# Kernel optimization log

Hardware: AMD Instinct MI355X
Metric: run time of the kernel (lower is better)

The kernel has to match this reference:

```python
import jax, jax.numpy as jnp
import numpy as np

DEPTH, HEADS, DIM_HEAD = 6, 8, 64
B, N, E = 2, 128, 160
NUM_ATOMS, NF = 100, 127
DIM = NF + 1                 # 128, node feature dim fed to transformer
INNER = HEADS * DIM_HEAD     # 512


def setup_inputs() -> dict:
    key = jax.random.key(0)
    ks = iter(jax.random.split(key, 40))
    f32 = jnp.float32
    def w(shape, scale=0.02):
        return jax.random.normal(next(ks), shape, dtype=f32) * scale
    inp = {
        "indices": jax.random.randint(next(ks), (B, N), 0, NUM_ATOMS),
        "coordinates": jax.random.normal(next(ks), (B, N, 3), dtype=f32),
        "bonds": jax.random.randint(next(ks), (E, 2), 0, N),
        "noise_level": jax.random.uniform(next(ks), (1,), dtype=f32),
        "atom_emb": w((NUM_ATOMS, NF), 1.0),
        "ln1_g": jnp.ones((DEPTH, DIM), f32), "ln1_b": jnp.zeros((DEPTH, DIM), f32),
        "Wq": w((DEPTH, DIM, INNER)), "bq": jnp.zeros((DEPTH, INNER), f32),
        "Wkv": w((DEPTH, DIM, 2 * INNER)), "bkv": jnp.zeros((DEPTH, 2 * INNER), f32),
        "We": w((DEPTH, 3, INNER)), "be": jnp.zeros((DEPTH, INNER), f32),
        "Wo": w((DEPTH, INNER, DIM)), "bo": jnp.zeros((DEPTH, DIM), f32),
        "Wg1": w((DEPTH, 3 * DIM, 1)),
        "ln2_g": jnp.ones((DEPTH, DIM), f32), "ln2_b": jnp.zeros((DEPTH, DIM), f32),
        "W1": w((DEPTH, DIM, 4 * DIM)), "b1": jnp.zeros((DEPTH, 4 * DIM), f32),
        "W2": w((DEPTH, 4 * DIM, DIM)), "b2": jnp.zeros((DEPTH, DIM), f32),
        "Wg2": w((DEPTH, 3 * DIM, 1)),
        "Wlin": w((DIM, 1)), "blin": jnp.zeros((1,), f32),
    }
    return inp


def _ln(x, g, b, eps=1e-5):
    m = jnp.mean(x, -1, keepdims=True)
    v = jnp.mean((x - m) ** 2, -1, keepdims=True)
    return (x - m) * jax.lax.rsqrt(v + eps) * g + b


def _gated_residual(x, res, Wg):
    # gate = sigmoid(Linear([x, res, x-res])); out = x*gate + res*(1-gate)
    gate = jax.nn.sigmoid(jnp.concatenate([x, res, x - res], -1) @ Wg)  # (B,N,1)
    return x * gate + res * (1.0 - gate)


def _forward(indices, bonds, coordinates, noise_level, atom_emb,
             ln1_g, ln1_b, Wq, bq, Wkv, bkv, We, be, Wo, bo, Wg1,
             ln2_g, ln2_b, W1, b1, W2, b2, Wg2, Wlin, blin):
    b, n = indices.shape
    # nodes_embedding: atom embedding + noise-level channel
    noise = jnp.broadcast_to(noise_level.reshape(1, 1, 1).astype(coordinates.dtype), (b, n, 1))
    nodes = jnp.concatenate([atom_emb[indices], noise], -1)  # (B,N,DIM)
    # edges_embedding: vectorized scatter of per-bond coordinate differences
    i, j = bonds[:, 0], bonds[:, 1]
    diff = coordinates[:, i] - coordinates[:, j]             # (B,E,3)
    edges = jnp.zeros((b, n, n, 3), coordinates.dtype)
    edges = edges.at[:, i, j].set(diff).at[:, j, i].set(-diff)

    scale = DIM_HEAD ** -0.5
    for l in range(DEPTH):
        # PreNorm + edge-biased attention (mask is all-ones -> no-op)
        xn = _ln(nodes, ln1_g[l], ln1_b[l])
        q = (xn @ Wq[l] + bq[l]).reshape(b, n, HEADS, DIM_HEAD)
        k, v = jnp.split(xn @ Wkv[l] + bkv[l], 2, -1)
        k = k.reshape(b, n, HEADS, DIM_HEAD)
        v = v.reshape(b, n, HEADS, DIM_HEAD)
        e = (edges @ We[l] + be[l]).reshape(b, n, n, HEADS, DIM_HEAD)
        kk = k[:, None] + e                                   # (B,i,j,H,D)
        vv = v[:, None] + e
        sim = jnp.einsum('bihd,bijhd->bijh', q, kk) * scale
        attn = jax.nn.softmax(sim, axis=2)                    # softmax over j
        out = jnp.einsum('bijh,bijhd->bihd', attn, vv).reshape(b, n, INNER)
        out = out @ Wo[l] + bo[l]
        nodes = _gated_residual(out, nodes, Wg1[l])
        # PreNorm + FeedForward (exact GELU, mult=4) + gated residual
        xn = _ln(nodes, ln2_g[l], ln2_b[l])
        ff = jax.nn.gelu(xn @ W1[l] + b1[l], approximate=False) @ W2[l] + b2[l]
        nodes = _gated_residual(ff, nodes, Wg2[l])
    return jnp.sum(nodes @ Wlin + blin)


def reference(indices, coordinates, bonds, noise_level, atom_emb,
              ln1_g, ln1_b, Wq, bq, Wkv, bkv, We, be, Wo, bo, Wg1,
              ln2_g, ln2_b, W1, b1, W2, b2, Wg2, Wlin, blin):
    return _forward(indices, bonds, coordinates, noise_level, atom_emb,
                    ln1_g, ln1_b, Wq, bq, Wkv, bkv, We, be, Wo, bo, Wg1,
                    ln2_g, ln2_b, W1, b1, W2, b2, Wg2, Wlin, blin)
```

## Files before the change

### kernel.cpp

```cpp
#include <hip/hip_runtime.h>
#include <hip/hip_fp16.h>
#include <math.h>

#define DEPTH 6
#define HEADS 8
#define BB    2
#define NN    128
#define EE    160
#define NF    127
#define DIMM  128
#define INNER 512
#define NNODE 256

__device__ __forceinline__ void gload16(const void* g, void* l) {
    __builtin_amdgcn_global_load_lds((const __attribute__((address_space(1))) void*)g,
                                     (__attribute__((address_space(3))) void*)l,
                                     16, 0, 0);
}

__device__ __forceinline__ void wait_vm0() { __builtin_amdgcn_s_waitcnt(0x0f70); }
__device__ __forceinline__ void wait_lgkm0() { __builtin_amdgcn_s_waitcnt(0xC07F); }

__device__ __forceinline__ void wstage16(const char* gslice, char* ldsslice, int ln) {
#pragma unroll
    for (int i = 0; i < 16; i++)
        gload16(gslice + i * 1024 + ln * 16, ldsslice + i * 1024);
}
__device__ __forceinline__ void wstage16s(const char* gslice, int rowstride,
                                          char* ldsslice, int ln) {
#pragma unroll
    for (int i = 0; i < 16; i++)
        gload16(gslice + (size_t)i * rowstride + ln * 16, ldsslice + i * 1024);
}

__device__ __forceinline__ void fma8h(float4& a0, float4& a1, float s, float4 raw) {
    const __half2* hp = (const __half2*)&raw;
    float2 p0 = __half22float2(hp[0]), p1 = __half22float2(hp[1]);
    float2 p2 = __half22float2(hp[2]), p3 = __half22float2(hp[3]);
    a0.x += s * p0.x; a0.y += s * p0.y; a0.z += s * p1.x; a0.w += s * p1.y;
    a1.x += s * p2.x; a1.y += s * p2.y; a1.z += s * p3.x; a1.w += s * p3.y;
}

__device__ __forceinline__ void gemv512(const float* act, const float* wbuf,
                                        float* s_part, int w, int ln) {
    float4 a0 = {0,0,0,0}, a1 = {0,0,0,0};
    const float4* w4 = (const float4*)wbuf;
#pragma unroll
    for (int r = 0; r < 16; r++)
        fma8h(a0, a1, act[w * 16 + r], w4[r * 64 + ln]);
    ((float4*)(s_part + w * 512))[ln * 2]     = a0;
    ((float4*)(s_part + w * 512))[ln * 2 + 1] = a1;
}

__device__ __forceinline__ void gemv128(const float* act, const float* wbuf,
                                        float* s_part, int w, int ln) {
    float2 acc = {0, 0};
#pragma unroll 8
    for (int r = 0; r < 64; r++) {
        float raw = wbuf[r * 64 + ln];
        __half2 h = *(__half2*)&raw;
        float2 p = __half22float2(h);
        float a = act[w * 64 + r];
        acc.x += a * p.x; acc.y += a * p.y;
    }
    s_part[w * 128 + ln * 2]     = acc.x;
    s_part[w * 128 + ln * 2 + 1] = acc.y;
}

__device__ __forceinline__ float block_reduce_sum_8w(float val, float* sbuf) {
#pragma unroll
    for (int off = 32; off > 0; off >>= 1) val += __shfl_xor(val, off, 64);
    int wave = threadIdx.x >> 6;
    if ((threadIdx.x & 63) == 0) sbuf[wave] = val;
    __syncthreads();
    float r = sbuf[0] + sbuf[1] + sbuf[2] + sbuf[3] + sbuf[4] + sbuf[5] + sbuf[6] + sbuf[7];
    __syncthreads();
    return r;
}

__device__ __forceinline__ float2 block_reduce_sum2_8w(float a, float b, float* sbuf16) {
#pragma unroll
    for (int off = 32; off > 0; off >>= 1) {
        a += __shfl_xor(a, off, 64);
        b += __shfl_xor(b, off, 64);
    }
    int wave = threadIdx.x >> 6;
    if ((threadIdx.x & 63) == 0) { sbuf16[2 * wave] = a; sbuf16[2 * wave + 1] = b; }
    __syncthreads();
    float ra = 0.0f, rb = 0.0f;
#pragma unroll
    for (int g = 0; g < 8; g++) { ra += sbuf16[2 * g]; rb += sbuf16[2 * g + 1]; }
    __syncthreads();
    float2 r; r.x = ra; r.y = rb;
    return r;
}


__global__ __launch_bounds__(512) void k_cvt(const float* Wq, const float* Wkv,
                                             const float* Wo, const float* W1,
                                             const float* W2,
                                             __half* hWq, __half* hWkv, __half* hWo,
                                             __half* hW1, __half* hW2,
                                             const float* blin, float* out) {
    if (blockIdx.x == 0 && threadIdx.x == 0) out[0] = 256.0f * blin[0];
    int g = blockIdx.x * 512 + threadIdx.x;
    const float4* src; __half* dst; int off;
    if (g < 98304)       { src = (const float4*)Wq;  dst = hWq;  off = g; }
    else if (g < 294912) { src = (const float4*)Wkv; dst = hWkv; off = g - 98304; }
    else if (g < 393216) { src = (const float4*)Wo;  dst = hWo;  off = g - 294912; }
    else if (g < 491520) { src = (const float4*)W1;  dst = hW1;  off = g - 393216; }
    else                 { src = (const float4*)W2;  dst = hW2;  off = g - 491520; }
    float4 v = src[off];
    __half2* d2 = (__half2*)(dst + (size_t)off * 4);
    d2[0] = __floats2half2_rn(v.x, v.y);
    d2[1] = __floats2half2_rn(v.z, v.w);
}

__global__ __launch_bounds__(512, 1) void k_pre(const int* indices, const float* noise,
                                                const float* atom_emb,
                                                const float* ln1_g, const float* ln1_b,
                                                const __half* hWq, const float* bq,
                                                const __half* hWkv, const float* bkv,
                                                float* nodes, float* qb,
                                                __half* hk, __half* hv) {
    int bn = blockIdx.x;
    int t  = threadIdx.x;
    int d  = t & 127;
    bool own = (t < 128);
    int w = t >> 6, ln = t & 63;
    __shared__ float arena[32768];
    __shared__ float s_xn[128];
    __shared__ float s_red[16];
    __shared__ float s_part[4096];
    char*  lslice = (char*)arena + w * 16384;
    float* wbuf   = arena + w * 4096;

    const char* WqL  = (const char*)(hWq + 0);
    const char* WkvL = (const char*)(hWkv + 0);
    wstage16(WqL + w * 16384, lslice, ln);

    float nd = 0.0f;
    if (own) {
        int idx = indices[bn];
        nd = (d < NF) ? atom_emb[idx * NF + d] : noise[0];
        nodes[bn * DIMM + d] = nd;
    }
    float2 ss = block_reduce_sum2_8w(own ? nd : 0.0f, own ? nd * nd : 0.0f, s_red);
    float m   = ss.x * (1.0f / 128.0f);
    float var = ss.y * (1.0f / 128.0f) - m * m;
    if (own) s_xn[d] = (nd - m) * rsqrtf(var + 1e-5f) * ln1_g[d] + ln1_b[d];
    __syncthreads();

    wait_vm0();
    gemv512(s_xn, wbuf, s_part, w, ln);
    wait_lgkm0();
    wstage16s(WkvL + (size_t)(w * 16) * 2048, 2048, lslice, ln);
    __syncthreads();
    {
        float q = bq[t];
#pragma unroll
        for (int g = 0; g < 8; g++) q += s_part[g * 512 + t];
        qb[(size_t)bn * INNER + t] = q;
    }
    __syncthreads();

    wait_vm0();
    gemv512(s_xn, wbuf, s_part, w, ln);
    wait_lgkm0();
    wstage16s(WkvL + (size_t)(w * 16) * 2048 + 1024, 2048, lslice, ln);
    __syncthreads();
    {
        float k = bkv[t];
#pragma unroll
        for (int g = 0; g < 8; g++) k += s_part[g * 512 + t];
        hk[(size_t)bn * INNER + t] = __float2half(k);
    }
    __syncthreads();

    wait_vm0();
    gemv512(s_xn, wbuf, s_part, w, ln);
    __syncthreads();
    {
        float v = bkv[INNER + t];
#pragma unroll
        for (int g = 0; g < 8; g++) v += s_part[g * 512 + t];
        hv[(size_t)bn * INNER + t] = __float2half(v);
    }
}

__global__ __launch_bounds__(512, 1) void k_layer(int l,
        const float* coords, const int* bonds,
        const float* We, const float* be,
        float* qb, const __half* hkin, const __half* hvin,
        __half* hkout, __half* hvout,
        const __half* hWo, const float* bo, const float* Wg1,
        const float* ln2_g, const float* ln2_b,
        const __half* hW1, const float* b1,
        const __half* hW2, const float* b2,
        const float* Wg2,
        const float* ln1_g, const float* ln1_b,
        const __half* hWq, const float* bq,
        const __half* hWkv, const float* bkv,
        float* nodes, const float* Wlin, float* out) {
    int bn = blockIdx.x;
    int b = bn >> 7, i = bn & 127;
    int t = threadIdx.x;
    int d = t & 127;
    bool own = (t < 128);
    int w = t >> 6, ln = t & 63;

    __shared__ float arena[32768];
    __shared__ float scoord[384];
    __shared__ float sedge[384];
    __shared__ int   sadj[128];
    __shared__ float s_l[64];
    __shared__ float s_ao[512];
    __shared__ float s_h[512];
    __shared__ float s_xn[128];
    __shared__ float s_red[16];
    __shared__ float s_part[4096];
    float* s_o = s_part;
    char*  lslice = (char*)arena + w * 16384;
    float* wbuf   = arena + w * 4096;

    const char* WoL  = (const char*)(hWo + (size_t)l * INNER * DIMM);
    const char* W1L  = (const char*)(hW1 + (size_t)l * DIMM * 4 * DIMM);
    const char* W2L  = (const char*)(hW2 + (size_t)l * 4 * DIMM * DIMM);
    const char* WqL  = (const char*)(hWq + (size_t)(l + 1) * DIMM * INNER);
    const char* WkvL = (const char*)(hWkv + (size_t)(l + 1) * DIMM * 2 * INNER);

    wstage16(WoL + w * 16384, lslice, ln);

    const float4* qR4 = (const float4*)(qb + (size_t)bn * INNER);
    const float4* WeR = (const float4*)(We + (size_t)l * 3 * INNER);
    float4 qa  = qR4[ln * 2],        qz  = qR4[ln * 2 + 1];
    float4 w0a = WeR[ln * 2],        w0z = WeR[ln * 2 + 1];
    float4 w1a = WeR[128 + ln * 2],  w1z = WeR[129 + ln * 2];
    float4 w2a = WeR[256 + ln * 2],  w2z = WeR[257 + ln * 2];
    float4 bea = ((const float4*)(be + (size_t)l * INNER))[ln * 2];
    float4 bez = ((const float4*)(be + (size_t)l * INNER))[ln * 2 + 1];
    float res = own ? nodes[bn * DIMM + d] : 0.0f;

    if (t < 3 * NN) scoord[t] = coords[b * 3 * NN + t];
    if (t < NN) sadj[t] = 0;
    __syncthreads();
    if (t < EE) {
        int e0 = bonds[2 * t], e1 = bonds[2 * t + 1];
        if (e0 == i) sadj[e1] = 1;
        if (e1 == i) sadj[e0] = 1;
    }
    __syncthreads();
    if (t < NN) {
        int j = t;
        float msk = sadj[j] ? 1.0f : 0.0f;
        sedge[3 * j + 0] = msk * (scoord[3 * i + 0] - scoord[3 * j + 0]);
        sedge[3 * j + 1] = msk * (scoord[3 * i + 1] - scoord[3 * j + 1]);
        sedge[3 * j + 2] = msk * (scoord[3 * i + 2] - scoord[3 * j + 2]);
    }
    __syncthreads();

    const float4* kR = (const float4*)(hkin + (size_t)b * NN * INNER);
    const float4* vR = (const float4*)(hvin + (size_t)b * NN * INNER);
    float l_run = 0.0f;
    float4 o0 = {0, 0, 0, 0}, o1 = {0, 0, 0, 0};
    int j0 = w * 16;
#pragma unroll
    for (int base = 0; base < 16; base += 4) {
        float4 kraw[4], vraw[4];
#pragma unroll
        for (int p = 0; p < 4; p++) {
            int j = j0 + base + p;
            kraw[p] = kR[j * 64 + ln];
            vraw[p] = vR[j * 64 + ln];
        }
#pragma unroll
        for (int p = 0; p < 4; p++) {
            int j = j0 + base + p;
            float ex = sedge[3 * j], ey = sedge[3 * j + 1], ez = sedge[3 * j + 2];
            float4 e0, e1;
            e0.x = bea.x + ex * w0a.x + ey * w1a.x + ez * w2a.x;
            e0.y = bea.y + ex * w0a.y + ey * w1a.y + ez * w2a.y;
            e0.z = bea.z + ex * w0a.z + ey * w1a.z + ez * w2a.z;
            e0.w = bea.w + ex * w0a.w + ey * w1a.w + ez * w2a.w;
            e1.x = bez.x + ex * w0z.x + ey * w1z.x + ez * w2z.x;
            e1.y = bez.y + ex * w0z.y + ey * w1z.y + ez * w2z.y;
            e1.z = bez.z + ex * w0z.z + ey * w1z.z + ez * w2z.z;
            e1.w = bez.w + ex * w0z.w + ey * w1z.w + ez * w2z.w;
            const __half2* kh = (const __half2*)&kraw[p];
            float2 k0 = __half22float2(kh[0]), k1 = __half22float2(kh[1]);
            float2 k2 = __half22float2(kh[2]), k3 = __half22float2(kh[3]);
            float s = qa.x * (k0.x + e0.x) + qa.y * (k0.y + e0.y)
                    + qa.z * (k1.x + e0.z) + qa.w * (k1.y + e0.w)
                    + qz.x * (k2.x + e1.x) + qz.y * (k2.y + e1.y)
                    + qz.z * (k3.x + e1.z) + qz.w * (k3.y + e1.w);
            s += __shfl_xor(s, 1, 64);
            s += __shfl_xor(s, 2, 64);
            s += __shfl_xor(s, 4, 64);
            float pp = __expf(s * 0.125f);
            const __half2* vh = (const __half2*)&vraw[p];
            float2 v0 = __half22float2(vh[0]), v1 = __half22float2(vh[1]);
            float2 v2 = __half22float2(vh[2]), v3 = __half22float2(vh[3]);
            l_run += pp;
            o0.x += pp * (v0.x + e0.x); o0.y += pp * (v0.y + e0.y);
            o0.z += pp * (v1.x + e0.z); o0.w += pp * (v1.y + e0.w);
            o1.x += pp * (v2.x + e1.x); o1.y += pp * (v2.y + e1.y);
            o1.z += pp * (v3.x + e1.z); o1.w += pp * (v3.y + e1.w);
        }
    }
    ((float4*)(s_o + w * 512))[ln * 2]     = o0;
    ((float4*)(s_o + w * 512))[ln * 2 + 1] = o1;
    if ((ln & 7) == 0) s_l[w * 8 + (ln >> 3)] = l_run;
    __syncthreads();
    {
        float o = 0.0f;
#pragma unroll
        for (int g = 0; g < 8; g++) o += s_o[g * 512 + t];
        int h = t >> 6;
        float lsum = 0.0f;
#pragma unroll
        for (int g = 0; g < 8; g++) lsum += s_l[g * 8 + h];
        s_ao[t] = o / lsum;
    }
    __syncthreads();

    wait_vm0();
    gemv128(s_ao, wbuf, s_part, w, ln);
    wait_lgkm0();
    wstage16(W1L + w * 16384, lslice, ln);
    __syncthreads();
    float x = 0.0f;
    if (own) {
        x = bo[l * DIMM + d];
#pragma unroll
        for (int g = 0; g < 8; g++) x += s_part[g * 128 + d];
    }
    __syncthreads();

    const float* Wg1_l = Wg1 + l * 3 * DIMM;
    float texpr = own ? (x * Wg1_l[d] + res * Wg1_l[DIMM + d] + (x - res) * Wg1_l[2 * DIMM + d]) : 0.0f;
    float g1 = block_reduce_sum_8w(texpr, s_red);
    g1 = 1.0f / (1.0f + __expf(-g1));
    float n1 = x * g1 + res * (1.0f - g1);

    float2 ss = block_reduce_sum2_8w(own ? n1 : 0.0f, own ? n1 * n1 : 0.0f, s_red);
    float m   = ss.x * (1.0f / 128.0f);
    float var = ss.y * (1.0f / 128.0f) - m * m;
    if (own) s_xn[d] = (n1 - m) * rsqrtf(var + 1e-5f) * ln2_g[l * DIMM + d] + ln2_b[l * DIMM + d];
    __syncthreads();

    wait_vm0();
    gemv512(s_xn, wbuf, s_part, w, ln);
    wait_lgkm0();
    wstage16(W2L + w * 16384, lslice, ln);
    __syncthreads();
    {
        float a = b1[l * 4 * DIMM + t];
#pragma unroll
        for (int g = 0; g < 8; g++) a += s_part[g * 512 + t];
        a = 0.5f * a * (1.0f + erff(a * 0.70710678f));
        s_h[t] = a;
    }
    __syncthreads();

    wait_vm0();
    gemv128(s_h, wbuf, s_part, w, ln);
    wait_lgkm0();
    if (l < DEPTH - 1) wstage16(WqL + w * 16384, lslice, ln);
    __syncthreads();
    float y = 0.0f;
    if (own) {
        y = b2[l * DIMM + d];
#pragma unroll
        for (int g = 0; g < 8; g++) y += s_part[g * 128 + d];
    }
    __syncthreads();

    const float* Wg2_l = Wg2 + l * 3 * DIMM;
    texpr = own ? (y * Wg2_l[d] + n1 * Wg2_l[DIMM + d] + (y - n1) * Wg2_l[2 * DIMM + d]) : 0.0f;
    float g2 = block_reduce_sum_8w(texpr, s_red);
    g2 = 1.0f / (1.0f + __expf(-g2));
    float n2 = y * g2 + n1 * (1.0f - g2);
    if (own) nodes[bn * DIMM + d] = n2;

    if (l < DEPTH - 1) {
        float2 s1 = block_reduce_sum2_8w(own ? n2 : 0.0f, own ? n2 * n2 : 0.0f, s_red);
        float m1   = s1.x * (1.0f / 128.0f);
        float var1 = s1.y * (1.0f / 128.0f) - m1 * m1;
        if (own) s_xn[d] = (n2 - m1) * rsqrtf(var1 + 1e-5f) * ln1_g[(l + 1) * DIMM + d]
                         + ln1_b[(l + 1) * DIMM + d];
        __syncthreads();

        wait_vm0();
        gemv512(s_xn, wbuf, s_part, w, ln);
        wait_lgkm0();
        wstage16s(WkvL + (size_t)(w * 16) * 2048, 2048, lslice, ln);
        __syncthreads();
        {
            float q = bq[(l + 1) * INNER + t];
#pragma unroll
            for (int g = 0; g < 8; g++) q += s_part[g * 512 + t];
            qb[(size_t)bn * INNER + t] = q;
        }
        __syncthreads();

        wait_vm0();
        gemv512(s_xn, wbuf, s_part, w, ln);
        wait_lgkm0();
        wstage16s(WkvL + (size_t)(w * 16) * 2048 + 1024, 2048, lslice, ln);
        __syncthreads();
        {
            float k = bkv[(l + 1) * 2 * INNER + t];
#pragma unroll
            for (int g = 0; g < 8; g++) k += s_part[g * 512 + t];
            hkout[(size_t)bn * INNER + t] = __float2half(k);
        }
        __syncthreads();

        wait_vm0();
        gemv512(s_xn, wbuf, s_part, w, ln);
        __syncthreads();
        {
            float v = bkv[(l + 1) * 2 * INNER + INNER + t];
#pragma unroll
            for (int g = 0; g < 8; g++) v += s_part[g * 512 + t];
            hvout[(size_t)bn * INNER + t] = __float2half(v);
        }
    } else {
        float contrib = own ? n2 * Wlin[d] : 0.0f;
        float tot = block_reduce_sum_8w(contrib, s_red);
        if (t == 0) atomicAdd(out, tot);
    }
}

extern "C" void kernel_launch(void* const* d_in, const int* in_sizes, int n_in,
                              void* d_out, int out_size, void* d_ws, size_t ws_size,
                              hipStream_t stream) {
    const int*   indices = (const int*)d_in[0];
    const float* coords  = (const float*)d_in[1];
    const int*   bonds   = (const int*)d_in[2];
    const float* noise   = (const float*)d_in[3];
    const float* atom_emb= (const float*)d_in[4];
    const float* ln1_g   = (const float*)d_in[5];
    const float* ln1_b   = (const float*)d_in[6];
    const float* Wq      = (const float*)d_in[7];
    const float* bq      = (const float*)d_in[8];
    const float* Wkv     = (const float*)d_in[9];
    const float* bkv     = (const float*)d_in[10];
    const float* We      = (const float*)d_in[11];
    const float* be      = (const float*)d_in[12];
    const float* Wo      = (const float*)d_in[13];
    const float* bo      = (const float*)d_in[14];
    const float* Wg1     = (const float*)d_in[15];
    const float* ln2_g   = (const float*)d_in[16];
    const float* ln2_b   = (const float*)d_in[17];
    const float* W1      = (const float*)d_in[18];
    const float* b1      = (const float*)d_in[19];
    const float* W2      = (const float*)d_in[20];
    const float* b2      = (const float*)d_in[21];
    const float* Wg2     = (const float*)d_in[22];
    const float* Wlin    = (const float*)d_in[23];
    const float* blin    = (const float*)d_in[24];

    float*  ws    = (float*)d_ws;
    float*  nodes = ws;
    float*  qb    = nodes + NNODE * DIMM;
    __half* hkb   = (__half*)(qb + NNODE * INNER);
    __half* hvb   = hkb + 2 * NNODE * INNER;
    __half* hWq   = hvb + 2 * NNODE * INNER;
    __half* hWkv  = hWq + DEPTH * DIMM * INNER;
    __half* hWo   = hWkv + DEPTH * DIMM * 2 * INNER;
    __half* hW1   = hWo + DEPTH * INNER * DIMM;
    __half* hW2   = hW1 + DEPTH * DIMM * 4 * DIMM;

    k_cvt<<<1152, 512, 0, stream>>>(Wq, Wkv, Wo, W1, W2, hWq, hWkv, hWo, hW1, hW2,
                                    blin, (float*)d_out);
    k_pre<<<NNODE, 512, 0, stream>>>(indices, noise, atom_emb, ln1_g, ln1_b,
                                     hWq, bq, hWkv, bkv, nodes, qb, hkb, hvb);
    for (int l = 0; l < DEPTH; l++) {
        const __half* hkin = hkb + (size_t)(l & 1) * NNODE * INNER;
        const __half* hvin = hvb + (size_t)(l & 1) * NNODE * INNER;
        __half* hkout = hkb + (size_t)((l + 1) & 1) * NNODE * INNER;
        __half* hvout = hvb + (size_t)((l + 1) & 1) * NNODE * INNER;
        k_layer<<<NNODE, 512, 0, stream>>>(l, coords, bonds, We, be,
                                           qb, hkin, hvin, hkout, hvout,
                                           hWo, bo, Wg1, ln2_g, ln2_b, hW1, b1, hW2, b2,
                                           Wg2, ln1_g, ln1_b, hWq, bq, hWkv, bkv,
                                           nodes, Wlin, (float*)d_out);
    }
}
```

Baseline: 267.0 us.

## Use column-striped GEMV staging and fuse gate and layernorm reductions

The 512-wide GEMVs now give each wave its own 64-column stripe. A half-wave shuffle reduction replaces the cross-wave s_part buffer, which removes several block barriers per projection. The gated-residual gate and the following layernorm statistics are computed in one multi-value block reduction by expanding the mean and variance algebraically in the gate value. The bond mask is now built by a per-thread scan over all edges instead of a scatter into an adjacency array. The edge scan adds 160 iterations per thread, and the algebraic variance may lose some precision.

Measured after the change: 342.2 us. 28.2% more time.

```diff
diff --git a/kernel.cpp b/kernel.cpp
--- a/kernel.cpp
+++ b/kernel.cpp
@@ -26,40 +26,39 @@
     for (int i = 0; i < 16; i++)
         gload16(gslice + i * 1024 + ln * 16, ldsslice + i * 1024);
 }
-__device__ __forceinline__ void wstage16s(const char* gslice, int rowstride,
-                                          char* ldsslice, int ln) {
+
+__device__ __forceinline__ void wstage_stripe(const char* gcolbase, int rowstride,
+                                              char* ldsslice, int ln) {
 #pragma unroll
     for (int i = 0; i < 16; i++)
-        gload16(gslice + (size_t)i * rowstride + ln * 16, ldsslice + i * 1024);
-}
-
-__device__ __forceinline__ void fma8h(float4& a0, float4& a1, float s, float4 raw) {
-    const __half2* hp = (const __half2*)&raw;
-    float2 p0 = __half22float2(hp[0]), p1 = __half22float2(hp[1]);
-    float2 p2 = __half22float2(hp[2]), p3 = __half22float2(hp[3]);
-    a0.x += s * p0.x; a0.y += s * p0.y; a0.z += s * p1.x; a0.w += s * p1.y;
-    a1.x += s * p2.x; a1.y += s * p2.y; a1.z += s * p3.x; a1.w += s * p3.y;
-}
-
-__device__ __forceinline__ void gemv512(const float* act, const float* wbuf,
-                                        float* s_part, int w, int ln) {
-    float4 a0 = {0,0,0,0}, a1 = {0,0,0,0};
-    const float4* w4 = (const float4*)wbuf;
-#pragma unroll
-    for (int r = 0; r < 16; r++)
-        fma8h(a0, a1, act[w * 16 + r], w4[r * 64 + ln]);
-    ((float4*)(s_part + w * 512))[ln * 2]     = a0;
-    ((float4*)(s_part + w * 512))[ln * 2 + 1] = a1;
+        gload16(gcolbase + (size_t)(i * 8 + (ln >> 3)) * rowstride + (ln & 7) * 16,
+                ldsslice + i * 1024);
+}
+
+__device__ __forceinline__ float2 gemv512cs(const float* act, const float* wbuf, int ln) {
+    int p = ln & 31, rh = ln >> 5;
+    const float* base = wbuf + rh * 64 * 32;
+    const float* a    = act + rh * 64;
+    float2 acc = {0.0f, 0.0f};
+#pragma unroll 8
+    for (int k = 0; k < 64; k++) {
+        float raw = base[k * 32 + p];
+        float2 pr = __half22float2(*(const __half2*)&raw);
+        acc.x += a[k] * pr.x;
+        acc.y += a[k] * pr.y;
+    }
+    acc.x += __shfl_xor(acc.x, 32, 64);
+    acc.y += __shfl_xor(acc.y, 32, 64);
+    return acc;
 }
 
 __device__ __forceinline__ void gemv128(const float* act, const float* wbuf,
                                         float* s_part, int w, int ln) {
-    float2 acc = {0, 0};
+    float2 acc = {0.0f, 0.0f};
 #pragma unroll 8
     for (int r = 0; r < 64; r++) {
         float raw = wbuf[r * 64 + ln];
-        __half2 h = *(__half2*)&raw;
-        float2 p = __half22float2(h);
+        float2 p = __half22float2(*(const __half2*)&raw);
         float a = act[w * 64 + r];
         acc.x += a * p.x; acc.y += a * p.y;
     }
@@ -67,32 +66,29 @@
     s_part[w * 128 + ln * 2 + 1] = acc.y;
 }
 
-__device__ __forceinline__ float block_reduce_sum_8w(float val, float* sbuf) {
-#pragma unroll
-    for (int off = 32; off > 0; off >>= 1) val += __shfl_xor(val, off, 64);
+template <int N>
+__device__ __forceinline__ void block_reduce_n(float* vals, float* sbuf) {
+#pragma unroll
+    for (int off = 32; off > 0; off >>= 1)
+#pragma unroll
+        for (int q = 0; q < N; q++) vals[q] += __shfl_xor(vals[q], off, 64);
     int wave = threadIdx.x >> 6;
-    if ((threadIdx.x & 63) == 0) sbuf[wave] = val;
-    __syncthreads();
-    float r = sbuf[0] + sbuf[1] + sbuf[2] + sbuf[3] + sbuf[4] + sbuf[5] + sbuf[6] + sbuf[7];
-    __syncthreads();
-    return r;
-}
-
-__device__ __forceinline__ float2 block_reduce_sum2_8w(float a, float b, float* sbuf16) {
-#pragma unroll
-    for (int off = 32; off > 0; off >>= 1) {
-        a += __shfl_xor(a, off, 64);
-        b += __shfl_xor(b, off, 64);
-    }
-    int wave = threadIdx.x >> 6;
-    if ((threadIdx.x & 63) == 0) { sbuf16[2 * wave] = a; sbuf16[2 * wave + 1] = b; }
-    __syncthreads();
-    float ra = 0.0f, rb = 0.0f;
-#pragma unroll
-    for (int g = 0; g < 8; g++) { ra += sbuf16[2 * g]; rb += sbuf16[2 * g + 1]; }
-    __syncthreads();
-    float2 r; r.x = ra; r.y = rb;
-    return r;
+    if ((threadIdx.x & 63) == 0)
+#pragma unroll
+        for (int q = 0; q < N; q++) sbuf[wave * N + q] = vals[q];
+    __syncthreads();
+#pragma unroll
+    for (int q = 0; q < N; q++) {
+        float r = 0.0f;
+#pragma unroll
+        for (int g = 0; g < 8; g++) r += sbuf[g * N + q];
+        vals[q] = r;
+    }
+    __syncthreads();
+}
+
+__device__ __forceinline__ float gelu_exact(float a) {
+    return 0.5f * a * (1.0f + erff(a * 0.70710678f));
 }
 
 
@@ -130,14 +126,13 @@
     int w = t >> 6, ln = t & 63;
     __shared__ float arena[32768];
     __shared__ float s_xn[128];
-    __shared__ float s_red[16];
-    __shared__ float s_part[4096];
+    __shared__ float s_red[48];
     char*  lslice = (char*)arena + w * 16384;
     float* wbuf   = arena + w * 4096;
 
-    const char* WqL  = (const char*)(hWq + 0);
-    const char* WkvL = (const char*)(hWkv + 0);
-    wstage16(WqL + w * 16384, lslice, ln);
+    const char* WqL  = (const char*)hWq;
+    const char* WkvL = (const char*)hWkv;
+    wstage_stripe(WqL + w * 128, 1024, lslice, ln);
 
     float nd = 0.0f;
     if (own) {
@@ -145,47 +140,38 @@
         nd = (d < NF) ? atom_emb[idx * NF + d] : noise[0];
         nodes[bn * DIMM + d] = nd;
     }
-    float2 ss = block_reduce_sum2_8w(own ? nd : 0.0f, own ? nd * nd : 0.0f, s_red);
-    float m   = ss.x * (1.0f / 128.0f);
-    float var = ss.y * (1.0f / 128.0f) - m * m;
+    float vals[2] = {own ? nd : 0.0f, own ? nd * nd : 0.0f};
+    block_reduce_n<2>(vals, s_red);
+    float m   = vals[0] * (1.0f / 128.0f);
+    float var = vals[1] * (1.0f / 128.0f) - m * m;
     if (own) s_xn[d] = (nd - m) * rsqrtf(var + 1e-5f) * ln1_g[d] + ln1_b[d];
     __syncthreads();
 
-    wait_vm0();
-    gemv512(s_xn, wbuf, s_part, w, ln);
+    int p = ln & 31;
+    int cg = w * 64 + 2 * p;
+
+    wait_vm0();
+    float2 q2 = gemv512cs(s_xn, wbuf, ln);
     wait_lgkm0();
-    wstage16s(WkvL + (size_t)(w * 16) * 2048, 2048, lslice, ln);
-    __syncthreads();
-    {
-        float q = bq[t];
-#pragma unroll
-        for (int g = 0; g < 8; g++) q += s_part[g * 512 + t];
-        qb[(size_t)bn * INNER + t] = q;
-    }
-    __syncthreads();
-
-    wait_vm0();
-    gemv512(s_xn, wbuf, s_part, w, ln);
+    wstage_stripe(WkvL + w * 128, 2048, lslice, ln);
+    if (ln < 32) {
+        float2 o; o.x = q2.x + bq[cg]; o.y = q2.y + bq[cg + 1];
+        ((float2*)(qb + (size_t)bn * INNER))[w * 32 + p] = o;
+    }
+
+    wait_vm0();
+    float2 k2 = gemv512cs(s_xn, wbuf, ln);
     wait_lgkm0();
-    wstage16s(WkvL + (size_t)(w * 16) * 2048 + 1024, 2048, lslice, ln);
-    __syncthreads();
-    {
-        float k = bkv[t];
-#pragma unroll
-        for (int g = 0; g < 8; g++) k += s_part[g * 512 + t];
-        hk[(size_t)bn * INNER + t] = __float2half(k);
-    }
-    __syncthreads();
-
-    wait_vm0();
-    gemv512(s_xn, wbuf, s_part, w, ln);
-    __syncthreads();
-    {
-        float v = bkv[INNER + t];
-#pragma unroll
-        for (int g = 0; g < 8; g++) v += s_part[g * 512 + t];
-        hv[(size_t)bn * INNER + t] = __float2half(v);
-    }
+    wstage_stripe(WkvL + 1024 + w * 128, 2048, lslice, ln);
+    if (ln < 32)
+        ((__half2*)(hk + (size_t)bn * INNER))[w * 32 + p] =
+            __floats2half2_rn(k2.x + bkv[cg], k2.y + bkv[cg + 1]);
+
+    wait_vm0();
+    float2 v2 = gemv512cs(s_xn, wbuf, ln);
+    if (ln < 32)
+        ((__half2*)(hv + (size_t)bn * INNER))[w * 32 + p] =
+            __floats2half2_rn(v2.x + bkv[INNER + cg], v2.y + bkv[INNER + cg + 1]);
 }
 
 __global__ __launch_bounds__(512, 1) void k_layer(int l,
@@ -212,12 +198,12 @@
     __shared__ float arena[32768];
     __shared__ float scoord[384];
     __shared__ float sedge[384];
-    __shared__ int   sadj[128];
+    __shared__ int   sbonds[2 * EE];
     __shared__ float s_l[64];
     __shared__ float s_ao[512];
     __shared__ float s_h[512];
     __shared__ float s_xn[128];
-    __shared__ float s_red[16];
+    __shared__ float s_red[48];
     __shared__ float s_part[4096];
     float* s_o = s_part;
     char*  lslice = (char*)arena + w * 16384;
@@ -241,18 +227,16 @@
     float4 bez = ((const float4*)(be + (size_t)l * INNER))[ln * 2 + 1];
     float res = own ? nodes[bn * DIMM + d] : 0.0f;
 
+    if (t < 2 * EE) sbonds[t] = bonds[t];
     if (t < 3 * NN) scoord[t] = coords[b * 3 * NN + t];
-    if (t < NN) sadj[t] = 0;
-    __syncthreads();
-    if (t < EE) {
-        int e0 = bonds[2 * t], e1 = bonds[2 * t + 1];
-        if (e0 == i) sadj[e1] = 1;
-        if (e1 == i) sadj[e0] = 1;
-    }
     __syncthreads();
     if (t < NN) {
         int j = t;
-        float msk = sadj[j] ? 1.0f : 0.0f;
+        float msk = 0.0f;
+        for (int e = 0; e < EE; e++) {
+            int e0 = sbonds[2 * e], e1 = sbonds[2 * e + 1];
+            if ((e0 == i && e1 == j) || (e1 == i && e0 == j)) msk = 1.0f;
+        }
         sedge[3 * j + 0] = msk * (scoord[3 * i + 0] - scoord[3 * j + 0]);
         sedge[3 * j + 1] = msk * (scoord[3 * i + 1] - scoord[3 * j + 1]);
         sedge[3 * j + 2] = msk * (scoord[3 * i + 2] - scoord[3 * j + 2]);
@@ -326,7 +310,7 @@
     wait_vm0();
     gemv128(s_ao, wbuf, s_part, w, ln);
     wait_lgkm0();
-    wstage16(W1L + w * 16384, lslice, ln);
+    wstage_stripe(W1L + w * 128, 1024, lslice, ln);
     __syncthreads();
     float x = 0.0f;
     if (own) {
@@ -334,38 +318,47 @@
 #pragma unroll
         for (int g = 0; g < 8; g++) x += s_part[g * 128 + d];
     }
-    __syncthreads();
 
     const float* Wg1_l = Wg1 + l * 3 * DIMM;
-    float texpr = own ? (x * Wg1_l[d] + res * Wg1_l[DIMM + d] + (x - res) * Wg1_l[2 * DIMM + d]) : 0.0f;
-    float g1 = block_reduce_sum_8w(texpr, s_red);
-    g1 = 1.0f / (1.0f + __expf(-g1));
-    float n1 = x * g1 + res * (1.0f - g1);
-
-    float2 ss = block_reduce_sum2_8w(own ? n1 : 0.0f, own ? n1 * n1 : 0.0f, s_red);
-    float m   = ss.x * (1.0f / 128.0f);
-    float var = ss.y * (1.0f / 128.0f) - m * m;
-    if (own) s_xn[d] = (n1 - m) * rsqrtf(var + 1e-5f) * ln2_g[l * DIMM + d] + ln2_b[l * DIMM + d];
-    __syncthreads();
-
-    wait_vm0();
-    gemv512(s_xn, wbuf, s_part, w, ln);
-    wait_lgkm0();
-    wstage16(W2L + w * 16384, lslice, ln);
-    __syncthreads();
     {
-        float a = b1[l * 4 * DIMM + t];
-#pragma unroll
-        for (int g = 0; g < 8; g++) a += s_part[g * 512 + t];
-        a = 0.5f * a * (1.0f + erff(a * 0.70710678f));
-        s_h[t] = a;
+        float tex = own ? (x * Wg1_l[d] + res * Wg1_l[DIMM + d] + (x - res) * Wg1_l[2 * DIMM + d]) : 0.0f;
+        float vals[6] = {tex,
+                         own ? x : 0.0f, own ? x * x : 0.0f,
+                         own ? x * res : 0.0f,
+                         own ? res : 0.0f, own ? res * res : 0.0f};
+        block_reduce_n<6>(vals, s_red);
+        float g1 = 1.0f / (1.0f + __expf(-vals[0]));
+        float sn  = g1 * vals[1] + (1.0f - g1) * vals[4];
+        float sn2 = g1 * g1 * vals[2] + 2.0f * g1 * (1.0f - g1) * vals[3]
+                  + (1.0f - g1) * (1.0f - g1) * vals[5];
+        float m   = sn * (1.0f / 128.0f);
+        float var = sn2 * (1.0f / 128.0f) - m * m;
+        float n1v = x * g1 + res * (1.0f - g1);
+        res = n1v;
+        if (own) s_xn[d] = (n1v - m) * rsqrtf(var + 1e-5f) * ln2_g[l * DIMM + d] + ln2_b[l * DIMM + d];
+    }
+    __syncthreads();
+    float n1 = res;
+
+    wait_vm0();
+    {
+        float2 a2 = gemv512cs(s_xn, wbuf, ln);
+        wait_lgkm0();
+        wstage16(W2L + w * 16384, lslice, ln);
+        if (ln < 32) {
+            int p = ln & 31, cg = w * 64 + 2 * p;
+            float2 o;
+            o.x = gelu_exact(a2.x + b1[l * 4 * DIMM + cg]);
+            o.y = gelu_exact(a2.y + b1[l * 4 * DIMM + cg + 1]);
+            ((float2*)s_h)[w * 32 + p] = o;
+        }
     }
     __syncthreads();
 
     wait_vm0();
     gemv128(s_h, wbuf, s_part, w, ln);
     wait_lgkm0();
-    if (l < DEPTH - 1) wstage16(WqL + w * 16384, lslice, ln);
+    if (l < DEPTH - 1) wstage_stripe(WqL + w * 128, 1024, lslice, ln);
     __syncthreads();
     float y = 0.0f;
     if (own) {
@@ -373,61 +366,65 @@
 #pragma unroll
         for (int g = 0; g < 8; g++) y += s_part[g * 128 + d];
     }
-    __syncthreads();
 
     const float* Wg2_l = Wg2 + l * 3 * DIMM;
-    texpr = own ? (y * Wg2_l[d] + n1 * Wg2_l[DIMM + d] + (y - n1) * Wg2_l[2 * DIMM + d]) : 0.0f;
-    float g2 = block_reduce_sum_8w(texpr, s_red);
-    g2 = 1.0f / (1.0f + __expf(-g2));
-    float n2 = y * g2 + n1 * (1.0f - g2);
-    if (own) nodes[bn * DIMM + d] = n2;
-
     if (l < DEPTH - 1) {
-        float2 s1 = block_reduce_sum2_8w(own ? n2 : 0.0f, own ? n2 * n2 : 0.0f, s_red);
-        float m1   = s1.x * (1.0f / 128.0f);
-        float var1 = s1.y * (1.0f / 128.0f) - m1 * m1;
-        if (own) s_xn[d] = (n2 - m1) * rsqrtf(var1 + 1e-5f) * ln1_g[(l + 1) * DIMM + d]
-                         + ln1_b[(l + 1) * DIMM + d];
+        float tex = own ? (y * Wg2_l[d] + n1 * Wg2_l[DIMM + d] + (y - n1) * Wg2_l[2 * DIMM + d]) : 0.0f;
+        float vals[6] = {tex,
+                         own ? y : 0.0f, own ? y * y : 0.0f,
+                         own ? y * n1 : 0.0f,
+                         own ? n1 : 0.0f, own ? n1 * n1 : 0.0f};
+        block_reduce_n<6>(vals, s_red);
+        float g2 = 1.0f / (1.0f + __expf(-vals[0]));
+        float sn  = g2 * vals[1] + (1.0f - g2) * vals[4];
+        float sn2 = g2 * g2 * vals[2] + 2.0f * g2 * (1.0f - g2) * vals[3]
+                  + (1.0f - g2) * (1.0f - g2) * vals[5];
+        float m   = sn * (1.0f / 128.0f);
+        float var = sn2 * (1.0f / 128.0f) - m * m;
+        float n2 = y * g2 + n1 * (1.0f - g2);
+        if (own) {
+            nodes[bn * DIMM + d] = n2;
+            s_xn[d] = (n2 - m) * rsqrtf(var + 1e-5f) * ln1_g[(l + 1) * DIMM + d]
+                    + ln1_b[(l + 1) * DIMM + d];
+        }
         __syncthreads();
 
+        int p = ln & 31;
+        int cg = w * 64 + 2 * p;
+
         wait_vm0();
-        gemv512(s_xn, wbuf, s_part, w, ln);
+        float2 q2 = gemv512cs(s_xn, wbuf, ln);
         wait_lgkm0();
-        wstage16s(WkvL + (size_t)(w * 16) * 2048, 2048, lslice, ln);
-        __syncthreads();
-        {
-            float q = bq[(l + 1) * INNER + t];
-#pragma unroll
-            for (int g = 0; g < 8; g++) q += s_part[g * 512 + t];
-            qb[(size_t)bn * INNER + t] = q;
-        }
-        __syncthreads();
+        wstage_stripe(WkvL + w * 128, 2048, lslice, ln);
+        if (ln < 32) {
+            float2 o;
+            o.x = q2.x + bq[(l + 1) * INNER + cg];
+            o.y = q2.y + bq[(l + 1) * INNER + cg + 1];
+            ((float2*)(qb + (size_t)bn * INNER))[w * 32 + p] = o;
+        }
 
         wait_vm0();
-        gemv512(s_xn, wbuf, s_part, w, ln);
+        float2 k2 = gemv512cs(s_xn, wbuf, ln);
         wait_lgkm0();
-        wstage16s(WkvL + (size_t)(w * 16) * 2048 + 1024, 2048, lslice, ln);
-        __syncthreads();
-        {
-            float k = bkv[(l + 1) * 2 * INNER + t];
-#pragma unroll
-            for (int g = 0; g < 8; g++) k += s_part[g * 512 + t];
-            hkout[(size_t)bn * INNER + t] = __float2half(k);
-        }
-        __syncthreads();
+        wstage_stripe(WkvL + 1024 + w * 128, 2048, lslice, ln);
+        if (ln < 32)
+            ((__half2*)(hkout + (size_t)bn * INNER))[w * 32 + p] =
+                __floats2half2_rn(k2.x + bkv[(l + 1) * 2 * INNER + cg],
+                                  k2.y + bkv[(l + 1) * 2 * INNER + cg + 1]);
 
         wait_vm0();
-        gemv512(s_xn, wbuf, s_part, w, ln);
-        __syncthreads();
-        {
-            float v = bkv[(l + 1) * 2 * INNER + INNER + t];
-#pragma unroll
-            for (int g = 0; g < 8; g++) v += s_part[g * 512 + t];
-            hvout[(size_t)bn * INNER + t] = __float2half(v);
-        }
+        float2 v2 = gemv512cs(s_xn, wbuf, ln);
+        if (ln < 32)
+            ((__half2*)(hvout + (size_t)bn * INNER))[w * 32 + p] =
+                __floats2half2_rn(v2.x + bkv[(l + 1) * 2 * INNER + INNER + cg],
+                                  v2.y + bkv[(l + 1) * 2 * INNER + INNER + cg + 1]);
     } else {
-        float contrib = own ? n2 * Wlin[d] : 0.0f;
-        float tot = block_reduce_sum_8w(contrib, s_red);
+        float wl = own ? Wlin[d] : 0.0f;
+        float tex = own ? (y * Wg2_l[d] + n1 * Wg2_l[DIMM + d] + (y - n1) * Wg2_l[2 * DIMM + d]) : 0.0f;
+        float vals[3] = {tex, y * wl, n1 * wl};
+        block_reduce_n<3>(vals, s_red);
+        float g2 = 1.0f / (1.0f + __expf(-vals[0]));
+        float tot = g2 * vals[1] + (1.0f - g2) * vals[2];
         if (t == 0) atomicAdd(out, tot);
     }
 }
```
